# Performance work log

Measured on AMD Instinct MI355X. Metric: run time of the kernel, lower is better.

## Reference

```python
import jax, jax.numpy as jnp
import numpy as np

N_WRD = 2000
WCODE = 3
EMB = 32
VSIZE = 7
VIEW = (16, 16)
B = 64
CSIZE = 128


def _vcode():
    # torch.meshgrid with default 'ij' indexing, cat -> (2, H*W) -> (H*W, 2)
    x = jnp.linspace(-1.0, 1.0, VIEW[0])
    y = jnp.linspace(-1.0, 1.0, VIEW[1])
    xg, yg = jnp.meshgrid(x, y, indexing='ij')
    return jnp.stack([xg.reshape(-1), yg.reshape(-1)], axis=-1)  # (V, 2)


def setup_inputs() -> dict:
    key = jax.random.key(0)
    ks = jax.random.split(key, 20)
    s = 0.02
    d = {
        'view_cell': jax.random.normal(ks[0], (B, CSIZE, VIEW[0] * VIEW[1]), jnp.float32),
        'v': jax.random.normal(ks[1], (B, VSIZE), jnp.float32),
        'w2c_w1': jax.random.normal(ks[2], (VSIZE, 512), jnp.float32) * s,
        'w2c_b1': jnp.zeros((512,), jnp.float32),
        'w2c_w2': jax.random.normal(ks[3], (512, WCODE * N_WRD), jnp.float32) * s,
        'w2c_b2': jnp.zeros((WCODE * N_WRD,), jnp.float32),
        'fc1_w': jax.random.normal(ks[4], (WCODE, 256), jnp.float32) * s,
        'fc1_b': jnp.zeros((256,), jnp.float32),
        'fc2_w': jax.random.normal(ks[5], (256, 256), jnp.float32) * s,
        'fc2_b': jnp.zeros((256,), jnp.float32),
        'fca_w': jax.random.normal(ks[6], (256, 1), jnp.float32) * s,
        'fca_b': jnp.zeros((1,), jnp.float32),
        'fce_w': jax.random.normal(ks[7], (256, EMB), jnp.float32) * s,
        'fce_b': jnp.zeros((EMB,), jnp.float32),
        'vse_w1': jax.random.normal(ks[8], (2, 128), jnp.float32) * s,
        'vse_b1': jnp.zeros((128,), jnp.float32),
        'vse_w2': jax.random.normal(ks[9], (128, EMB), jnp.float32) * s,
        'vse_b2': jnp.zeros((EMB,), jnp.float32),
    }
    return d


def reference(view_cell, v, w2c_w1, w2c_b1, w2c_w2, w2c_b2,
              fc1_w, fc1_b, fc2_w, fc2_b, fca_w, fca_b, fce_w, fce_b,
              vse_w1, vse_b1, vse_w2, vse_b2):
    b = v.shape[0]
    # w2c: v -> per-cell world codes
    h0 = jax.nn.relu(v @ w2c_w1 + w2c_b1)                     # (B, 512)
    wcode = (h0 @ w2c_w2 + w2c_b2).reshape(-1, WCODE)          # (B*N, 3)
    h = jax.nn.relu(wcode @ fc1_w + fc1_b)                     # (B*N, 256)
    h = jax.nn.relu(h @ fc2_w + fc2_b)
    activation = jax.nn.sigmoid(h @ fca_w + fca_b).reshape(b, N_WRD, 1)
    cs_emb = (h @ fce_w + fce_b).reshape(b, N_WRD, EMB)        # (B, N, E)
    # view-space embedding of the pixel grid
    vcode = _vcode()                                           # (V, 2)
    vs = jax.nn.relu(vcode @ vse_w1 + vse_b1) @ vse_w2 + vse_b2  # (V, E)
    # relation / gated softmax routing
    relation = jnp.einsum('bne,ve->bnv', cs_emb, vs)           # (B, N, V)
    route = jax.nn.softmax(relation, axis=2) * activation      # (B, N, V)
    # write: view_cell (B, C, V) @ route^T (B, V, N) -> (B, C, N)
    wrd_cell = jnp.einsum('bcv,bnv->bcn', view_cell, route)
    return wrd_cell
```

## Files before the change

### kernel.cpp

```cpp
#include <hip/hip_runtime.h>
#include <hip/hip_bf16.h>
#include <math.h>

#define NWRD 2000
#define BB 64
#define CS 128
#define VV 256

typedef __attribute__((ext_vector_type(8)))  short short8;
typedef __attribute__((ext_vector_type(16))) float f32x16;

#define WS_FC2WT 0
#define WS_WCODE (WS_FC2WT + 32768)
#define WS_VSB   (WS_WCODE + 384000)
#define WS_VCB   (WS_VSB + 4096)
#define WS_FCEWT (WS_VCB + 1048576)
#define WS_FCAWB (WS_FCEWT + 4096)

__device__ __forceinline__ unsigned short f2bf(float x) {
    unsigned int u = __float_as_uint(x);
    u += 0x7fffu + ((u >> 16) & 1u);
    return (unsigned short)(u >> 16);
}

#define PL_A 1024
#define PL_B (PL_A + 32)
#define PL_C (PL_B + 16)
#define PL_N (PL_C + 1)
__global__ __launch_bounds__(256) void kprep_light(
        const float* __restrict__ vc, unsigned short* __restrict__ vcb,
        const float* __restrict__ vse_w1, const float* __restrict__ vse_b1,
        const float* __restrict__ vse_w2, const float* __restrict__ vse_b2,
        unsigned short* __restrict__ vsb,
        const float* __restrict__ fc2_w, unsigned short* __restrict__ fc2wT,
        const float* __restrict__ fce_w, unsigned short* __restrict__ fcewT,
        const float* __restrict__ fca_w, unsigned short* __restrict__ fcawB) {
    __shared__ unsigned short smem[9216];
    int bid = blockIdx.x, t = threadIdx.x;
    if (bid < PL_A) {
        int i = (bid * 256 + t) * 8;
        float4 f0 = *(const float4*)(vc + i);
        float4 f1 = *(const float4*)(vc + i + 4);
        union { short8 v8; unsigned short u[8]; } o;
        o.u[0] = f2bf(f0.x); o.u[1] = f2bf(f0.y); o.u[2] = f2bf(f0.z); o.u[3] = f2bf(f0.w);
        o.u[4] = f2bf(f1.x); o.u[5] = f2bf(f1.y); o.u[6] = f2bf(f1.z); o.u[7] = f2bf(f1.w);
        *(short8*)(vcb + i) = o.v8;
    } else if (bid < PL_B) {
        float* hs = (float*)smem;
        int blk = bid - PL_A;
        int m = t & 127, half = t >> 7;
#pragma unroll
        for (int q = 0; q < 4; q++) {
            int vloc = half*4 + q;
            int vv = blk*8 + vloc;
            float x = (2.f/15.f)*(float)(vv >> 4) - 1.f;
            float y = (2.f/15.f)*(float)(vv & 15) - 1.f;
            float h = vse_b1[m] + x*vse_w1[m] + y*vse_w1[128 + m];
            hs[vloc*128 + m] = fmaxf(h, 0.f);
        }
        __syncthreads();
        int vloc = t >> 5, e = t & 31;
        float s = vse_b2[e];
        for (int mm = 0; mm < 128; mm++) s = fmaf(hs[vloc*128 + mm], vse_w2[mm*32 + e], s);
        vsb[(blk*8 + vloc)*32 + e] = f2bf(s);
    } else if (bid < PL_C) {
        unsigned short (*tile)[72] = (unsigned short(*)[72])smem;
        int b2 = bid - PL_B;
        int k0t = (b2 >> 2) * 64, n0t = (b2 & 3) * 64;
        int nl = t & 63, kb = (t >> 6) * 16;
#pragma unroll
        for (int i = 0; i < 16; i++)
            tile[kb + i][nl] = f2bf(fc2_w[(size_t)(k0t + kb + i)*256 + n0t + nl]);
        __syncthreads();
        int kl = t & 63, nb = (t >> 6) * 16;
#pragma unroll
        for (int i = 0; i < 16; i++)
            fc2wT[(size_t)(n0t + nb + i)*256 + k0t + kl] = tile[kl][nb + i];
    } else {
        int e = t & 31, kb = (t >> 5) * 32;
        unsigned short tmp[32];
#pragma unroll
        for (int i = 0; i < 32; i++) tmp[i] = f2bf(fce_w[(size_t)(kb + i)*32 + e]);
#pragma unroll
        for (int i = 0; i < 4; i++)
            *(short8*)(fcewT + (size_t)e*256 + kb + i*8) = *(short8*)(tmp + i*8);
#pragma unroll
        for (int i = 0; i < 32; i++)
            fcawB[(size_t)e*256 + kb + i] = (e == 0) ? f2bf(fca_w[kb + i]) : (unsigned short)0;
    }
}

#define W2_LDS (64*520*2*2)
__global__ __launch_bounds__(256) void kprep_w2(
        const float* __restrict__ w2, const float* __restrict__ v,
        const float* __restrict__ w2c_w1, const float* __restrict__ w2c_b1,
        const float* __restrict__ w2c_b2, float* __restrict__ wcode) {
    extern __shared__ char plds[];
    unsigned short* h0L = (unsigned short*)plds;
    unsigned short* w2L = (unsigned short*)(plds + 64*520*2);
    int t = threadIdx.x;
    int n0 = blockIdx.x * 64;
    {
        int nl = t & 63, kq = t >> 6;
        int ncl = (n0 + nl) < 6000 ? (n0 + nl) : 5999;
#pragma unroll 4
        for (int k = kq*128; k < kq*128 + 128; k += 2) {
            unsigned int p = (unsigned int)f2bf(w2[(size_t)k*6000 + ncl])
                           | ((unsigned int)f2bf(w2[(size_t)(k+1)*6000 + ncl]) << 16);
            *(unsigned int*)(w2L + nl*520 + k) = p;
        }
    }
    {
        int j0 = t * 2;
        float wk0[7], wk1[7];
#pragma unroll
        for (int k = 0; k < 7; k++) { wk0[k] = w2c_w1[k*512 + j0]; wk1[k] = w2c_w1[k*512 + j0 + 1]; }
        float bb0 = w2c_b1[j0], bb1 = w2c_b1[j0 + 1];
        for (int b = 0; b < 64; b++) {
            float s0 = bb0, s1 = bb1;
#pragma unroll
            for (int k = 0; k < 7; k++) {
                float vv = v[b*7 + k];
                s0 = fmaf(vv, wk0[k], s0);
                s1 = fmaf(vv, wk1[k], s1);
            }
            unsigned int p = (unsigned int)f2bf(fmaxf(s0, 0.f))
                           | ((unsigned int)f2bf(fmaxf(s1, 0.f)) << 16);
            *(unsigned int*)(h0L + b*520 + j0) = p;
        }
    }
    __syncthreads();
    int w = t >> 6, lane = t & 63, l31 = lane & 31, h = lane >> 5;
    int mt = w & 1, nt = w >> 1;
    f32x16 acc;
#pragma unroll
    for (int i = 0; i < 16; i++) acc[i] = 0.f;
#pragma unroll 8
    for (int ks = 0; ks < 32; ks++) {
        int k0 = ks*16 + h*8;
        short8 af = *(const short8*)(h0L + (mt*32 + l31)*520 + k0);
        short8 bf = *(const short8*)(w2L + (nt*32 + l31)*520 + k0);
        acc = __builtin_amdgcn_mfma_f32_32x32x16_bf16(af, bf, acc, 0, 0, 0);
    }
    int n = n0 + nt*32 + l31;
    if (n < 6000) {
        float bias = w2c_b2[n];
#pragma unroll
        for (int i = 0; i < 16; i++) {
            int row = (i & 3) + 8*(i >> 2) + 4*h;
            wcode[(size_t)(mt*32 + row)*6000 + n] = acc[i] + bias;
        }
    }
}

#define K45_LDS 77056
__global__ __launch_bounds__(512, 4) void k45(
        const unsigned short* __restrict__ vcb,
        const float* __restrict__ wcode,
        const float* __restrict__ fc1_w, const float* __restrict__ fc1_b,
        const unsigned short* __restrict__ fc2wT, const float* __restrict__ fc2_b,
        const float* __restrict__ fca_b_p,
        const unsigned short* __restrict__ fcawB,
        const unsigned short* __restrict__ fcewT, const float* __restrict__ fce_b,
        const unsigned short* __restrict__ vsb,
        float* __restrict__ out) {
    extern __shared__ char lds[];
    unsigned short* h1b    = (unsigned short*)lds;
    unsigned short* h2b    = (unsigned short*)(lds + 33792);
    unsigned short* routeB = h2b;
    unsigned short* embL   = (unsigned short*)(lds + 67584);
    float* actL   = (float*)(lds + 72704);
    float* wcsAll = (float*)(lds + 72960);
    float* redS   = (float*)(lds + 76032);
    int t = threadIdx.x;
    int w = t >> 6, lane = t & 63, l31 = lane & 31, h = lane >> 5;
    int b = blockIdx.y;
    int n0 = blockIdx.x * 256;

    {
        const float* wb = wcode + (size_t)b*6000;
        int i0 = n0*3 + t;
        wcsAll[t] = wb[i0 < 6000 ? i0 : 5999];
        if (t < 256) {
            int i1 = n0*3 + 512 + t;
            wcsAll[512 + t] = wb[i1 < 6000 ? i1 : 5999];
        }
    }
    int jq = (t & 63) * 4;
    float4 wa  = *(const float4*)(fc1_w + jq);
    float4 wb4 = *(const float4*)(fc1_w + 256 + jq);
    float4 wc  = *(const float4*)(fc1_w + 512 + jq);
    float4 bb4 = *(const float4*)(fc1_b + jq);
    int mtA = w & 1, na = (w >> 1) * 32, nb2 = na + 128;
    float ba = fc2_b[na + l31], bbv = fc2_b[nb2 + l31];
    float be = fce_b[l31];
    float fcab = fca_b_p[0];
    int ntR = w & 1, vq = w >> 1;
    int ctE = w >> 1, ntE = w & 1;
    size_t arowE = ((size_t)(b*128 + ctE*32 + l31))*256;
    __syncthreads();

    for (int c = 0; c < 4; c++) {
        int w0 = n0 + c*64;
#pragma unroll
        for (int rr = 0; rr < 8; rr++) {
            int r = w*8 + rr;
            const float* wr = wcsAll + (c*64 + r)*3;
            float c0 = wr[0], c1 = wr[1], c2 = wr[2];
            float v0 = fmaxf(fmaf(c2, wc.x, fmaf(c1, wb4.x, fmaf(c0, wa.x, bb4.x))), 0.f);
            float v1 = fmaxf(fmaf(c2, wc.y, fmaf(c1, wb4.y, fmaf(c0, wa.y, bb4.y))), 0.f);
            float v2 = fmaxf(fmaf(c2, wc.z, fmaf(c1, wb4.z, fmaf(c0, wa.z, bb4.z))), 0.f);
            float v3 = fmaxf(fmaf(c2, wc.w, fmaf(c1, wb4.w, fmaf(c0, wa.w, bb4.w))), 0.f);
            uint2 p;
            p.x = (unsigned int)f2bf(v0) | ((unsigned int)f2bf(v1) << 16);
            p.y = (unsigned int)f2bf(v2) | ((unsigned int)f2bf(v3) << 16);
            *(uint2*)(h1b + r*264 + jq) = p;
        }
        __syncthreads();
        {
            f32x16 c0, c1;
#pragma unroll
            for (int i = 0; i < 16; i++) { c0[i] = 0.f; c1[i] = 0.f; }
#pragma unroll 4
            for (int ks = 0; ks < 16; ks++) {
                int k0 = ks*16 + h*8;
                short8 af  = *(const short8*)(h1b + (mtA*32 + l31)*264 + k0);
                short8 bfa = *(const short8*)(fc2wT + (size_t)(na  + l31)*256 + k0);
                short8 bfb = *(const short8*)(fc2wT + (size_t)(nb2 + l31)*256 + k0);
                c0 = __builtin_amdgcn_mfma_f32_32x32x16_bf16(af, bfa, c0, 0, 0, 0);
                c1 = __builtin_amdgcn_mfma_f32_32x32x16_bf16(af, bfb, c1, 0, 0, 0);
            }
#pragma unroll
            for (int i = 0; i < 16; i++) {
                int row = (i & 3) + 8*(i >> 2) + 4*h;
                h2b[(mtA*32 + row)*264 + na  + l31] = f2bf(fmaxf(c0[i] + ba, 0.f));
                h2b[(mtA*32 + row)*264 + nb2 + l31] = f2bf(fmaxf(c1[i] + bbv, 0.f));
            }
        }
        __syncthreads();
        if (w < 2) {
            f32x16 ce;
#pragma unroll
            for (int i = 0; i < 16; i++) ce[i] = 0.f;
#pragma unroll 4
            for (int ks = 0; ks < 16; ks++) {
                int k0 = ks*16 + h*8;
                short8 af = *(const short8*)(h2b + (w*32 + l31)*264 + k0);
                short8 bf = *(const short8*)(fcewT + (size_t)l31*256 + k0);
                ce = __builtin_amdgcn_mfma_f32_32x32x16_bf16(af, bf, ce, 0, 0, 0);
            }
#pragma unroll
            for (int i = 0; i < 16; i++) {
                int row = (i & 3) + 8*(i >> 2) + 4*h;
                embL[(w*32 + row)*40 + l31] = f2bf(ce[i] + be);
            }
        } else if (w < 4) {
            int m = w - 2;
            f32x16 ca;
#pragma unroll
            for (int i = 0; i < 16; i++) ca[i] = 0.f;
#pragma unroll 4
            for (int ks = 0; ks < 16; ks++) {
                int k0 = ks*16 + h*8;
                short8 af = *(const short8*)(h2b + (m*32 + l31)*264 + k0);
                short8 bf = *(const short8*)(fcawB + (size_t)l31*256 + k0);
                ca = __builtin_amdgcn_mfma_f32_32x32x16_bf16(af, bf, ca, 0, 0, 0);
            }
            if (l31 == 0) {
#pragma unroll
                for (int i = 0; i < 16; i++) {
                    int row = (i & 3) + 8*(i >> 2) + 4*h;
                    actL[m*32 + row] = 1.f / (1.f + __expf(-(ca[i] + fcab)));
                }
            }
        }
        __syncthreads();
        int nloc = ntR*32 + l31;
        f32x16 ra[2];
#pragma unroll
        for (int mt = 0; mt < 2; mt++)
#pragma unroll
            for (int i = 0; i < 16; i++) ra[mt][i] = 0.f;
#pragma unroll
        for (int s = 0; s < 2; s++) {
            short8 bfrag = *(const short8*)(embL + nloc*40 + s*16 + h*8);
#pragma unroll
            for (int mt = 0; mt < 2; mt++) {
                int vrow = (vq*2 + mt)*32 + l31;
                short8 afrag = *(const short8*)(vsb + vrow*32 + s*16 + h*8);
                ra[mt] = __builtin_amdgcn_mfma_f32_32x32x16_bf16(afrag, bfrag, ra[mt], 0, 0, 0);
            }
        }
        float sm = 0.f;
#pragma unroll
        for (int mt = 0; mt < 2; mt++)
#pragma unroll
            for (int i = 0; i < 16; i++) {
                float e = __expf(ra[mt][i]);
                ra[mt][i] = e;
                sm += e;
            }
        sm += __shfl_xor(sm, 32);
        if (lane < 32) redS[w*32 + l31] = sm;
#pragma unroll
        for (int mt = 0; mt < 2; mt++) {
#pragma unroll
            for (int rp = 0; rp < 4; rp++) {
                int vb = (vq*2 + mt)*32 + rp*8 + h*4;
                unsigned int p0 = (unsigned int)f2bf(ra[mt][rp*4+0])
                                | ((unsigned int)f2bf(ra[mt][rp*4+1]) << 16);
                unsigned int p1 = (unsigned int)f2bf(ra[mt][rp*4+2])
                                | ((unsigned int)f2bf(ra[mt][rp*4+3]) << 16);
                *(uint2*)(routeB + nloc*264 + vb) = make_uint2(p0, p1);
            }
        }
        __syncthreads();
        {
            f32x16 cc;
#pragma unroll
            for (int i = 0; i < 16; i++) cc[i] = 0.f;
            const unsigned short* rrow = routeB + (ntE*32 + l31)*264;
#pragma unroll 4
            for (int ks = 0; ks < 16; ks++) {
                int k0 = ks*16 + h*8;
                short8 bf = *(const short8*)(rrow + k0);
                short8 a0 = *(const short8*)(vcb + arowE + k0);
                cc = __builtin_amdgcn_mfma_f32_32x32x16_bf16(a0, bf, cc, 0, 0, 0);
            }
            float ssum = redS[ntE*32 + l31] + redS[(2 + ntE)*32 + l31]
                       + redS[(4 + ntE)*32 + l31] + redS[(6 + ntE)*32 + l31];
            float scl = actL[ntE*32 + l31] / ssum;
            int ng = w0 + ntE*32 + l31;
            if (ng < NWRD) {
                float* ob = out + (size_t)b*128*NWRD + ng;
#pragma unroll
                for (int i = 0; i < 16; i++) {
                    int crow = (i & 3) + 8*(i >> 2) + 4*h;
                    ob[(size_t)(ctE*32 + crow)*NWRD] = cc[i] * scl;
                }
            }
        }
    }
}

extern "C" void kernel_launch(void* const* d_in, const int* in_sizes, int n_in,
                              void* d_out, int out_size, void* d_ws, size_t ws_size,
                              hipStream_t stream) {
    const float* view_cell = (const float*)d_in[0];
    const float* v       = (const float*)d_in[1];
    const float* w2c_w1  = (const float*)d_in[2];
    const float* w2c_b1  = (const float*)d_in[3];
    const float* w2c_w2  = (const float*)d_in[4];
    const float* w2c_b2  = (const float*)d_in[5];
    const float* fc1_w   = (const float*)d_in[6];
    const float* fc1_b   = (const float*)d_in[7];
    const float* fc2_w   = (const float*)d_in[8];
    const float* fc2_b   = (const float*)d_in[9];
    const float* fca_w   = (const float*)d_in[10];
    const float* fca_b   = (const float*)d_in[11];
    const float* fce_w   = (const float*)d_in[12];
    const float* fce_b   = (const float*)d_in[13];
    const float* vse_w1  = (const float*)d_in[14];
    const float* vse_b1  = (const float*)d_in[15];
    const float* vse_w2  = (const float*)d_in[16];
    const float* vse_b2  = (const float*)d_in[17];
    float* ws    = (float*)d_ws;
    unsigned short* fc2wT = (unsigned short*)(ws + WS_FC2WT);
    float* wcode = ws + WS_WCODE;
    unsigned short* vsb   = (unsigned short*)(ws + WS_VSB);
    unsigned short* vcb   = (unsigned short*)(ws + WS_VCB);
    unsigned short* fcewT = (unsigned short*)(ws + WS_FCEWT);
    unsigned short* fcawB = (unsigned short*)(ws + WS_FCAWB);
    float* out   = (float*)d_out;

    kprep_light<<<PL_N, 256, 0, stream>>>(view_cell, vcb,
                                          vse_w1, vse_b1, vse_w2, vse_b2, vsb,
                                          fc2_w, fc2wT, fce_w, fcewT, fca_w, fcawB);
    (void)hipFuncSetAttribute((const void*)kprep_w2,
                              hipFuncAttributeMaxDynamicSharedMemorySize, W2_LDS);
    kprep_w2<<<94, 256, W2_LDS, stream>>>(w2c_w2, v, w2c_w1, w2c_b1, w2c_b2, wcode);
    (void)hipFuncSetAttribute((const void*)k45,
                              hipFuncAttributeMaxDynamicSharedMemorySize, K45_LDS);
    dim3 g45(8, 64);
    k45<<<g45, 512, K45_LDS, stream>>>(vcb, wcode, fc1_w, fc1_b, fc2wT, fc2_b,
                                       fca_b, fcawB, fcewT, fce_b, vsb, out);
}
```

Measured before the change: 244.6 us.

## Fold fce projection with view-space embedding into single relation weight matrix

```diff
diff --git a/kernel.cpp b/kernel.cpp
--- a/kernel.cpp
+++ b/kernel.cpp
@@ -12,10 +12,9 @@
 
 #define WS_FC2WT 0
 #define WS_WCODE (WS_FC2WT + 32768)
-#define WS_VSB   (WS_WCODE + 384000)
-#define WS_VCB   (WS_VSB + 4096)
-#define WS_FCEWT (WS_VCB + 1048576)
-#define WS_FCAWB (WS_FCEWT + 4096)
+#define WS_WRELT (WS_WCODE + 384000)
+#define WS_CB    (WS_WRELT + 36864)
+#define WS_VCB   (WS_CB + 288)
 
 __device__ __forceinline__ unsigned short f2bf(float x) {
     unsigned int u = __float_as_uint(x);
@@ -24,18 +23,17 @@
 }
 
 #define PL_A 1024
-#define PL_B (PL_A + 32)
-#define PL_C (PL_B + 16)
-#define PL_N (PL_C + 1)
+#define PL_B (PL_A + 16)
+#define PL_N (PL_B + 9)
 __global__ __launch_bounds__(256) void kprep_light(
         const float* __restrict__ vc, unsigned short* __restrict__ vcb,
+        const float* __restrict__ fc2_w, unsigned short* __restrict__ fc2wT,
         const float* __restrict__ vse_w1, const float* __restrict__ vse_b1,
         const float* __restrict__ vse_w2, const float* __restrict__ vse_b2,
-        unsigned short* __restrict__ vsb,
-        const float* __restrict__ fc2_w, unsigned short* __restrict__ fc2wT,
-        const float* __restrict__ fce_w, unsigned short* __restrict__ fcewT,
-        const float* __restrict__ fca_w, unsigned short* __restrict__ fcawB) {
-    __shared__ unsigned short smem[9216];
+        const float* __restrict__ fce_w, const float* __restrict__ fce_b,
+        const float* __restrict__ fca_w,
+        unsigned short* __restrict__ WrelT, float* __restrict__ cb) {
+    __shared__ char sm[33792];
     int bid = blockIdx.x, t = threadIdx.x;
     if (bid < PL_A) {
         int i = (bid * 256 + t) * 8;
@@ -46,26 +44,8 @@
         o.u[4] = f2bf(f1.x); o.u[5] = f2bf(f1.y); o.u[6] = f2bf(f1.z); o.u[7] = f2bf(f1.w);
         *(short8*)(vcb + i) = o.v8;
     } else if (bid < PL_B) {
-        float* hs = (float*)smem;
-        int blk = bid - PL_A;
-        int m = t & 127, half = t >> 7;
-#pragma unroll
-        for (int q = 0; q < 4; q++) {
-            int vloc = half*4 + q;
-            int vv = blk*8 + vloc;
-            float x = (2.f/15.f)*(float)(vv >> 4) - 1.f;
-            float y = (2.f/15.f)*(float)(vv & 15) - 1.f;
-            float h = vse_b1[m] + x*vse_w1[m] + y*vse_w1[128 + m];
-            hs[vloc*128 + m] = fmaxf(h, 0.f);
-        }
-        __syncthreads();
-        int vloc = t >> 5, e = t & 31;
-        float s = vse_b2[e];
-        for (int mm = 0; mm < 128; mm++) s = fmaf(hs[vloc*128 + mm], vse_w2[mm*32 + e], s);
-        vsb[(blk*8 + vloc)*32 + e] = f2bf(s);
-    } else if (bid < PL_C) {
-        unsigned short (*tile)[72] = (unsigned short(*)[72])smem;
-        int b2 = bid - PL_B;
+        unsigned short (*tile)[72] = (unsigned short(*)[72])sm;
+        int b2 = bid - PL_A;
         int k0t = (b2 >> 2) * 64, n0t = (b2 & 3) * 64;
         int nl = t & 63, kb = (t >> 6) * 16;
 #pragma unroll
@@ -77,16 +57,45 @@
         for (int i = 0; i < 16; i++)
             fc2wT[(size_t)(n0t + nb + i)*256 + k0t + kl] = tile[kl][nb + i];
     } else {
-        int e = t & 31, kb = (t >> 5) * 32;
-        unsigned short tmp[32];
-#pragma unroll
-        for (int i = 0; i < 32; i++) tmp[i] = f2bf(fce_w[(size_t)(kb + i)*32 + e]);
-#pragma unroll
-        for (int i = 0; i < 4; i++)
-            *(short8*)(fcewT + (size_t)e*256 + kb + i*8) = *(short8*)(tmp + i*8);
-#pragma unroll
-        for (int i = 0; i < 32; i++)
-            fcawB[(size_t)e*256 + kb + i] = (e == 0) ? f2bf(fca_w[kb + i]) : (unsigned short)0;
+        int wb = bid - PL_B;
+        if (wb < 8) {
+            float* vsL = (float*)sm;
+            {
+                int v = t;
+                float x = (2.f/15.f)*(float)(v >> 4) - 1.f;
+                float y = (2.f/15.f)*(float)(v & 15) - 1.f;
+                float se[32];
+#pragma unroll
+                for (int e = 0; e < 32; e++) se[e] = vse_b2[e];
+                for (int m = 0; m < 128; m++) {
+                    float h = fmaxf(vse_b1[m] + x*vse_w1[m] + y*vse_w1[128 + m], 0.f);
+#pragma unroll
+                    for (int e = 0; e < 32; e++) se[e] = fmaf(h, vse_w2[m*32 + e], se[e]);
+                }
+#pragma unroll
+                for (int e = 0; e < 32; e++) vsL[v*33 + e] = se[e];
+                if (wb == 0) {
+                    float cbv = 0.f;
+#pragma unroll
+                    for (int e = 0; e < 32; e++) cbv = fmaf(fce_b[e], se[e], cbv);
+                    cb[v] = cbv;
+                }
+            }
+            __syncthreads();
+            int v = wb*32 + (t >> 3);
+            int k0 = (t & 7) * 32;
+            for (int k = k0; k < k0 + 32; k++) {
+                float s = 0.f;
+#pragma unroll
+                for (int e = 0; e < 32; e++) s = fmaf(fce_w[(size_t)k*32 + e], vsL[v*33 + e], s);
+                WrelT[(size_t)v*256 + k] = f2bf(s);
+            }
+        } else {
+            int k = t;
+            WrelT[(size_t)256*256 + k] = f2bf(fca_w[k]);
+            for (int r = 257; r < 288; r++) WrelT[(size_t)r*256 + k] = 0;
+            if (t < 32) cb[256 + t] = 0.f;
+        }
     }
 }
 
@@ -153,193 +162,159 @@
     }
 }
 
-#define K45_LDS 77056
-__global__ __launch_bounds__(512, 4) void k45(
+#define K45_LDS 37632
+__global__ __launch_bounds__(512, 8) void k45(
         const unsigned short* __restrict__ vcb,
         const float* __restrict__ wcode,
         const float* __restrict__ fc1_w, const float* __restrict__ fc1_b,
         const unsigned short* __restrict__ fc2wT, const float* __restrict__ fc2_b,
         const float* __restrict__ fca_b_p,
-        const unsigned short* __restrict__ fcawB,
-        const unsigned short* __restrict__ fcewT, const float* __restrict__ fce_b,
-        const unsigned short* __restrict__ vsb,
+        const unsigned short* __restrict__ WrelT, const float* __restrict__ cb,
         float* __restrict__ out) {
     extern __shared__ char lds[];
     unsigned short* h1b    = (unsigned short*)lds;
-    unsigned short* h2b    = (unsigned short*)(lds + 33792);
+    unsigned short* h2b    = (unsigned short*)(lds + 16896);
     unsigned short* routeB = h2b;
-    unsigned short* embL   = (unsigned short*)(lds + 67584);
-    float* actL   = (float*)(lds + 72704);
-    float* wcsAll = (float*)(lds + 72960);
-    float* redS   = (float*)(lds + 76032);
+    float* wcsAll = (float*)(lds + 33792);
+    float* redS   = (float*)(lds + 35328);
+    float* actL   = (float*)(lds + 36352);
+    float* cbL    = (float*)(lds + 36480);
     int t = threadIdx.x;
     int w = t >> 6, lane = t & 63, l31 = lane & 31, h = lane >> 5;
     int b = blockIdx.y;
-    int n0 = blockIdx.x * 256;
+    int n0 = blockIdx.x * 128;
+
+    if (t < 384) {
+        int idx = n0*3 + t;
+        wcsAll[t] = wcode[(size_t)b*6000 + (idx < 6000 ? idx : 5999)];
+    }
+    if (t < 288) cbL[t] = cb[t];
+    int jq = (t & 127) * 2, rb = t >> 7;
+    int ncol = w*32 + l31;
+    float ba = fc2_b[ncol];
+    float fcab = fca_b_p[0];
+    const unsigned short* arel  = WrelT + (size_t)(w*32 + l31)*256;
+    const unsigned short* arel2 = WrelT + (size_t)(256 + l31)*256;
+    const unsigned short* avc   = vcb + ((size_t)(b*128 + w*32 + l31))*256;
+    __syncthreads();
 
     {
-        const float* wb = wcode + (size_t)b*6000;
-        int i0 = n0*3 + t;
-        wcsAll[t] = wb[i0 < 6000 ? i0 : 5999];
-        if (t < 256) {
-            int i1 = n0*3 + 512 + t;
-            wcsAll[512 + t] = wb[i1 < 6000 ? i1 : 5999];
-        }
-    }
-    int jq = (t & 63) * 4;
-    float4 wa  = *(const float4*)(fc1_w + jq);
-    float4 wb4 = *(const float4*)(fc1_w + 256 + jq);
-    float4 wc  = *(const float4*)(fc1_w + 512 + jq);
-    float4 bb4 = *(const float4*)(fc1_b + jq);
-    int mtA = w & 1, na = (w >> 1) * 32, nb2 = na + 128;
-    float ba = fc2_b[na + l31], bbv = fc2_b[nb2 + l31];
-    float be = fce_b[l31];
-    float fcab = fca_b_p[0];
-    int ntR = w & 1, vq = w >> 1;
-    int ctE = w >> 1, ntE = w & 1;
-    size_t arowE = ((size_t)(b*128 + ctE*32 + l31))*256;
+        float2 wa = *(const float2*)(fc1_w + jq);
+        float2 wb2 = *(const float2*)(fc1_w + 256 + jq);
+        float2 wc = *(const float2*)(fc1_w + 512 + jq);
+        float2 bb = *(const float2*)(fc1_b + jq);
+#pragma unroll
+        for (int rr = 0; rr < 8; rr++) {
+            int r = rb*8 + rr;
+            const float* wr = wcsAll + r*3;
+            float c0 = wr[0], c1 = wr[1], c2 = wr[2];
+            float v0 = fmaxf(fmaf(c2, wc.x, fmaf(c1, wb2.x, fmaf(c0, wa.x, bb.x))), 0.f);
+            float v1 = fmaxf(fmaf(c2, wc.y, fmaf(c1, wb2.y, fmaf(c0, wa.y, bb.y))), 0.f);
+            *(unsigned int*)(h1b + r*264 + jq) =
+                (unsigned int)f2bf(v0) | ((unsigned int)f2bf(v1) << 16);
+        }
+    }
     __syncthreads();
 
     for (int c = 0; c < 4; c++) {
-        int w0 = n0 + c*64;
-#pragma unroll
-        for (int rr = 0; rr < 8; rr++) {
-            int r = w*8 + rr;
-            const float* wr = wcsAll + (c*64 + r)*3;
-            float c0 = wr[0], c1 = wr[1], c2 = wr[2];
-            float v0 = fmaxf(fmaf(c2, wc.x, fmaf(c1, wb4.x, fmaf(c0, wa.x, bb4.x))), 0.f);
-            float v1 = fmaxf(fmaf(c2, wc.y, fmaf(c1, wb4.y, fmaf(c0, wa.y, bb4.y))), 0.f);
-            float v2 = fmaxf(fmaf(c2, wc.z, fmaf(c1, wb4.z, fmaf(c0, wa.z, bb4.z))), 0.f);
-            float v3 = fmaxf(fmaf(c2, wc.w, fmaf(c1, wb4.w, fmaf(c0, wa.w, bb4.w))), 0.f);
-            uint2 p;
-            p.x = (unsigned int)f2bf(v0) | ((unsigned int)f2bf(v1) << 16);
-            p.y = (unsigned int)f2bf(v2) | ((unsigned int)f2bf(v3) << 16);
-            *(uint2*)(h1b + r*264 + jq) = p;
-        }
-        __syncthreads();
         {
-            f32x16 c0, c1;
-#pragma unroll
-            for (int i = 0; i < 16; i++) { c0[i] = 0.f; c1[i] = 0.f; }
+            f32x16 acc;
+#pragma unroll
+            for (int i = 0; i < 16; i++) acc[i] = 0.f;
 #pragma unroll 4
             for (int ks = 0; ks < 16; ks++) {
                 int k0 = ks*16 + h*8;
-                short8 af  = *(const short8*)(h1b + (mtA*32 + l31)*264 + k0);
-                short8 bfa = *(const short8*)(fc2wT + (size_t)(na  + l31)*256 + k0);
-                short8 bfb = *(const short8*)(fc2wT + (size_t)(nb2 + l31)*256 + k0);
-                c0 = __builtin_amdgcn_mfma_f32_32x32x16_bf16(af, bfa, c0, 0, 0, 0);
-                c1 = __builtin_amdgcn_mfma_f32_32x32x16_bf16(af, bfb, c1, 0, 0, 0);
+                short8 af = *(const short8*)(h1b + l31*264 + k0);
+                short8 bf = *(const short8*)(fc2wT + (size_t)ncol*256 + k0);
+                acc = __builtin_amdgcn_mfma_f32_32x32x16_bf16(af, bf, acc, 0, 0, 0);
             }
 #pragma unroll
             for (int i = 0; i < 16; i++) {
                 int row = (i & 3) + 8*(i >> 2) + 4*h;
-                h2b[(mtA*32 + row)*264 + na  + l31] = f2bf(fmaxf(c0[i] + ba, 0.f));
-                h2b[(mtA*32 + row)*264 + nb2 + l31] = f2bf(fmaxf(c1[i] + bbv, 0.f));
-            }
-        }
-        __syncthreads();
-        if (w < 2) {
-            f32x16 ce;
-#pragma unroll
-            for (int i = 0; i < 16; i++) ce[i] = 0.f;
+                h2b[row*264 + ncol] = f2bf(fmaxf(acc[i] + ba, 0.f));
+            }
+        }
+        __syncthreads();
+        f32x16 ra, ra2;
+#pragma unroll
+        for (int i = 0; i < 16; i++) { ra[i] = 0.f; ra2[i] = 0.f; }
+#pragma unroll 4
+        for (int ks = 0; ks < 16; ks++) {
+            int k0 = ks*16 + h*8;
+            short8 bf = *(const short8*)(h2b + l31*264 + k0);
+            short8 af = *(const short8*)(arel + k0);
+            ra = __builtin_amdgcn_mfma_f32_32x32x16_bf16(af, bf, ra, 0, 0, 0);
+            if (w == 7) {
+                short8 af2 = *(const short8*)(arel2 + k0);
+                ra2 = __builtin_amdgcn_mfma_f32_32x32x16_bf16(af2, bf, ra2, 0, 0, 0);
+            }
+        }
+        {
+            float sm = 0.f;
+#pragma unroll
+            for (int i = 0; i < 16; i++) {
+                int vv = w*32 + (i & 3) + 8*(i >> 2) + 4*h;
+                float e = __expf(ra[i] + cbL[vv]);
+                ra[i] = e;
+                sm += e;
+            }
+            sm += __shfl_xor(sm, 32);
+            if (lane < 32) redS[w*32 + l31] = sm;
+            if (w == 7 && lane < 32)
+                actL[l31] = 1.f / (1.f + __expf(-(ra2[0] + fcab)));
+        }
+        __syncthreads();
+#pragma unroll
+        for (int rp = 0; rp < 4; rp++) {
+            int vb = w*32 + rp*8 + h*4;
+            *(unsigned int*)(routeB + l31*264 + vb) =
+                (unsigned int)f2bf(ra[rp*4+0]) | ((unsigned int)f2bf(ra[rp*4+1]) << 16);
+            *(unsigned int*)(routeB + l31*264 + vb + 2) =
+                (unsigned int)f2bf(ra[rp*4+2]) | ((unsigned int)f2bf(ra[rp*4+3]) << 16);
+        }
+        if (c < 3) {
+            float2 wa = *(const float2*)(fc1_w + jq);
+            float2 wb2 = *(const float2*)(fc1_w + 256 + jq);
+            float2 wc = *(const float2*)(fc1_w + 512 + jq);
+            float2 bb = *(const float2*)(fc1_b + jq);
+#pragma unroll
+            for (int rr = 0; rr < 8; rr++) {
+                int r = rb*8 + rr;
+                const float* wr = wcsAll + ((c+1)*32 + r)*3;
+                float c0 = wr[0], c1 = wr[1], c2 = wr[2];
+                float v0 = fmaxf(fmaf(c2, wc.x, fmaf(c1, wb2.x, fmaf(c0, wa.x, bb.x))), 0.f);
+                float v1 = fmaxf(fmaf(c2, wc.y, fmaf(c1, wb2.y, fmaf(c0, wa.y, bb.y))), 0.f);
+                *(unsigned int*)(h1b + r*264 + jq) =
+                    (unsigned int)f2bf(v0) | ((unsigned int)f2bf(v1) << 16);
+            }
+        }
+        __syncthreads();
+        if (w < 4) {
+            f32x16 cc;
+#pragma unroll
+            for (int i = 0; i < 16; i++) cc[i] = 0.f;
 #pragma unroll 4
             for (int ks = 0; ks < 16; ks++) {
                 int k0 = ks*16 + h*8;
-                short8 af = *(const short8*)(h2b + (w*32 + l31)*264 + k0);
-                short8 bf = *(const short8*)(fcewT + (size_t)l31*256 + k0);
-                ce = __builtin_amdgcn_mfma_f32_32x32x16_bf16(af, bf, ce, 0, 0, 0);
-            }
-#pragma unroll
-            for (int i = 0; i < 16; i++) {
-                int row = (i & 3) + 8*(i >> 2) + 4*h;
-                embL[(w*32 + row)*40 + l31] = f2bf(ce[i] + be);
-            }
-        } else if (w < 4) {
-            int m = w - 2;
-            f32x16 ca;
-#pragma unroll
-            for (int i = 0; i < 16; i++) ca[i] = 0.f;
-#pragma unroll 4
-            for (int ks = 0; ks < 16; ks++) {
-                int k0 = ks*16 + h*8;
-                short8 af = *(const short8*)(h2b + (m*32 + l31)*264 + k0);
-                short8 bf = *(const short8*)(fcawB + (size_t)l31*256 + k0);
-                ca = __builtin_amdgcn_mfma_f32_32x32x16_bf16(af, bf, ca, 0, 0, 0);
-            }
-            if (l31 == 0) {
-#pragma unroll
-                for (int i = 0; i < 16; i++) {
-                    int row = (i & 3) + 8*(i >> 2) + 4*h;
-                    actL[m*32 + row] = 1.f / (1.f + __expf(-(ca[i] + fcab)));
-                }
-            }
-        }
-        __syncthreads();
-        int nloc = ntR*32 + l31;
-        f32x16 ra[2];
-#pragma unroll
-        for (int mt = 0; mt < 2; mt++)
-#pragma unroll
-            for (int i = 0; i < 16; i++) ra[mt][i] = 0.f;
-#pragma unroll
-        for (int s = 0; s < 2; s++) {
-            short8 bfrag = *(const short8*)(embL + nloc*40 + s*16 + h*8);
-#pragma unroll
-            for (int mt = 0; mt < 2; mt++) {
-                int vrow = (vq*2 + mt)*32 + l31;
-                short8 afrag = *(const short8*)(vsb + vrow*32 + s*16 + h*8);
-                ra[mt] = __builtin_amdgcn_mfma_f32_32x32x16_bf16(afrag, bfrag, ra[mt], 0, 0, 0);
-            }
-        }
-        float sm = 0.f;
-#pragma unroll
-        for (int mt = 0; mt < 2; mt++)
-#pragma unroll
-            for (int i = 0; i < 16; i++) {
-                float e = __expf(ra[mt][i]);
-                ra[mt][i] = e;
-                sm += e;
-            }
-        sm += __shfl_xor(sm, 32);
-        if (lane < 32) redS[w*32 + l31] = sm;
-#pragma unroll
-        for (int mt = 0; mt < 2; mt++) {
-#pragma unroll
-            for (int rp = 0; rp < 4; rp++) {
-                int vb = (vq*2 + mt)*32 + rp*8 + h*4;
-                unsigned int p0 = (unsigned int)f2bf(ra[mt][rp*4+0])
-                                | ((unsigned int)f2bf(ra[mt][rp*4+1]) << 16);
-                unsigned int p1 = (unsigned int)f2bf(ra[mt][rp*4+2])
-                                | ((unsigned int)f2bf(ra[mt][rp*4+3]) << 16);
-                *(uint2*)(routeB + nloc*264 + vb) = make_uint2(p0, p1);
-            }
-        }
-        __syncthreads();
-        {
-            f32x16 cc;
-#pragma unroll
-            for (int i = 0; i < 16; i++) cc[i] = 0.f;
-            const unsigned short* rrow = routeB + (ntE*32 + l31)*264;
-#pragma unroll 4
-            for (int ks = 0; ks < 16; ks++) {
-                int k0 = ks*16 + h*8;
-                short8 bf = *(const short8*)(rrow + k0);
-                short8 a0 = *(const short8*)(vcb + arowE + k0);
-                cc = __builtin_amdgcn_mfma_f32_32x32x16_bf16(a0, bf, cc, 0, 0, 0);
-            }
-            float ssum = redS[ntE*32 + l31] + redS[(2 + ntE)*32 + l31]
-                       + redS[(4 + ntE)*32 + l31] + redS[(6 + ntE)*32 + l31];
-            float scl = actL[ntE*32 + l31] / ssum;
-            int ng = w0 + ntE*32 + l31;
+                short8 bf = *(const short8*)(routeB + l31*264 + k0);
+                short8 af = *(const short8*)(avc + k0);
+                cc = __builtin_amdgcn_mfma_f32_32x32x16_bf16(af, bf, cc, 0, 0, 0);
+            }
+            float ssum = 0.f;
+#pragma unroll
+            for (int q = 0; q < 8; q++) ssum += redS[q*32 + l31];
+            float scl = actL[l31] / ssum;
+            int ng = n0 + c*32 + l31;
             if (ng < NWRD) {
                 float* ob = out + (size_t)b*128*NWRD + ng;
 #pragma unroll
                 for (int i = 0; i < 16; i++) {
                     int crow = (i & 3) + 8*(i >> 2) + 4*h;
-                    ob[(size_t)(ctE*32 + crow)*NWRD] = cc[i] * scl;
+                    ob[(size_t)(w*32 + crow)*NWRD] = cc[i] * scl;
                 }
             }
         }
+        __syncthreads();
     }
 }
 
@@ -367,21 +342,20 @@
     float* ws    = (float*)d_ws;
     unsigned short* fc2wT = (unsigned short*)(ws + WS_FC2WT);
     float* wcode = ws + WS_WCODE;
-    unsigned short* vsb   = (unsigned short*)(ws + WS_VSB);
+    unsigned short* WrelT = (unsigned short*)(ws + WS_WRELT);
+    float* cb    = ws + WS_CB;
     unsigned short* vcb   = (unsigned short*)(ws + WS_VCB);
-    unsigned short* fcewT = (unsigned short*)(ws + WS_FCEWT);
-    unsigned short* fcawB = (unsigned short*)(ws + WS_FCAWB);
     float* out   = (float*)d_out;
 
-    kprep_light<<<PL_N, 256, 0, stream>>>(view_cell, vcb,
-                                          vse_w1, vse_b1, vse_w2, vse_b2, vsb,
-                                          fc2_w, fc2wT, fce_w, fcewT, fca_w, fcawB);
+    kprep_light<<<PL_N, 256, 0, stream>>>(view_cell, vcb, fc2_w, fc2wT,
+                                          vse_w1, vse_b1, vse_w2, vse_b2,
+                                          fce_w, fce_b, fca_w, WrelT, cb);
     (void)hipFuncSetAttribute((const void*)kprep_w2,
                               hipFuncAttributeMaxDynamicSharedMemorySize, W2_LDS);
     kprep_w2<<<94, 256, W2_LDS, stream>>>(w2c_w2, v, w2c_w1, w2c_b1, w2c_b2, wcode);
     (void)hipFuncSetAttribute((const void*)k45,
                               hipFuncAttributeMaxDynamicSharedMemorySize, K45_LDS);
-    dim3 g45(8, 64);
+    dim3 g45(16, 64);
     k45<<<g45, 512, K45_LDS, stream>>>(vcb, wcode, fc1_w, fc1_b, fc2wT, fc2_b,
-                                       fca_b, fcawB, fcewT, fce_b, vsb, out);
-}
+                                       fca_b, WrelT, cb, out);
+}
```

Result: slower. 368.9 us (+50.8%).
